# Performance work log

Measured on AMD Instinct MI355X. Metric: run time of the kernel, lower is better.

## Reference

```python
import jax, jax.numpy as jnp
import numpy as np

MIN_PTS = 4

def setup_inputs() -> dict:
    key = jax.random.key(0)
    ks = jax.random.split(key, 10)
    P, N = 2048, 256            # proposals, max points per proposal slot
    H1, H2, OUT = 64, 128, 256  # PointNet MLP widths, extractor out_dim
    points = jax.random.normal(ks[0], (P, N, 3), dtype=jnp.float32)
    lengths = jax.random.randint(ks[1], (P,), 0, N, dtype=jnp.int32)  # some < MIN_PTS -> invalid
    centers = jax.random.normal(ks[2], (P, 3), dtype=jnp.float32) * 10.0
    sizes = jax.random.uniform(ks[3], (P, 3), minval=0.5, maxval=4.0, dtype=jnp.float32)
    proposals = jnp.concatenate([centers, sizes], axis=1)  # (P, 6)
    def lin(k, fan_in, fan_out):
        return jax.random.normal(k, (fan_in, fan_out), dtype=jnp.float32) * np.float32(1.0 / np.sqrt(fan_in))
    return {
        'points': points, 'lengths': lengths, 'proposals': proposals,
        'W1': lin(ks[4], 3, H1),   'b1': jnp.zeros((H1,), jnp.float32),
        'W2': lin(ks[5], H1, H2),  'b2': jnp.zeros((H2,), jnp.float32),
        'W3': lin(ks[6], H2, OUT), 'b3': jnp.zeros((OUT,), jnp.float32),
        'Wc': lin(ks[7], OUT, 1),  'bc': jnp.zeros((1,), jnp.float32),
        'Wr': lin(ks[8], OUT, 4),  'br': jnp.zeros((4,), jnp.float32),
    }

def reference(points, lengths, proposals, W1, b1, W2, b2, W3, b3, Wc, bc, Wr, br):
    P, N, _ = points.shape
    # repeat-padding: point i of proposal p maps to index i % n_p (gather form of the torch loop)
    L = jnp.maximum(lengths, 1)
    idx = jnp.arange(N, dtype=lengths.dtype)[None, :] % L[:, None]          # (P, N)
    batched = jnp.take_along_axis(points, idx[:, :, None], axis=1)         # (P, N, 3)
    # MultiPositionExtractor: box-normalized coords -> pointwise MLP -> max-pool
    centers = proposals[:, :3]
    half = proposals[:, 3:] * 0.5 + 1e-6
    local = (batched - centers[:, None, :]) / half[:, None, :]             # (P, N, 3)
    h = jax.nn.relu(local @ W1 + b1)                                       # (P, N, 64)
    h = jax.nn.relu(h @ W2 + b2)                                           # (P, N, 128)
    h = jax.nn.relu(h @ W3 + b3)                                           # (P, N, 256)
    feats = jnp.max(h, axis=1)                                             # (P, 256)
    # scatter-back: proposals with < MIN_PTS points get zero feature vector
    valid = lengths >= MIN_PTS
    feats = jnp.where(valid[:, None], feats, jnp.zeros((), feats.dtype))
    cls_logits = feats @ Wc + bc                                           # (P, 1)
    reg_deltas = feats @ Wr + br                                           # (P, 4)
    return cls_logits, reg_deltas
```

## Files before the change

### kernel.cpp

```cpp
#include <hip/hip_runtime.h>
#include <hip/hip_bf16.h>

#define MIN_PTS 4

typedef short bf16x8 __attribute__((ext_vector_type(8)));
typedef float f32x4  __attribute__((ext_vector_type(4)));

__device__ __forceinline__ ushort f2bf(float x) {
    unsigned u = __float_as_uint(x);
    u = (u + 0x7fffu + ((u >> 16) & 1u)) >> 16;
    return (ushort)u;
}

__device__ __forceinline__ uint cvt_pk_bf16(float lo, float hi) {
    union { __hip_bfloat162 h; uint u; } cv;
    cv.h = __float22bfloat162_rn(make_float2(lo, hi));
    return cv.u;
}

__global__ void pack_weights(const float* __restrict__ W2, const float* __restrict__ W3,
                             ushort* __restrict__ B2P, ushort* __restrict__ B3P)
{
    int idx = blockIdx.x * 256 + threadIdx.x;
    if (idx < 8192) {
        int j = idx & 7, l = (idx >> 3) & 63, ks = (idx >> 9) & 1, nt = idx >> 10;
        int k   = ks * 32 + (l >> 4) * 8 + j;
        int col = nt * 16 + (l & 15);
        B2P[idx] = f2bf(W2[k * 128 + col]);
    }
    if (idx < 32768) {
        int j = idx & 7, l = (idx >> 3) & 63, ks = (idx >> 9) & 3, nt = idx >> 11;
        int k   = ks * 32 + (l >> 4) * 8 + j;
        int col = nt * 16 + (l & 15);
        B3P[idx] = f2bf(W3[k * 256 + col]);
    }
}

__global__ __launch_bounds__(512, 4) void refine_stripe128(
    const float* __restrict__ points,
    const int*   __restrict__ lengths,
    const float* __restrict__ proposals,
    const float* __restrict__ W1, const float* __restrict__ b1,
    const float* __restrict__ b2,
    const float* __restrict__ b3,
    const ushort* __restrict__ B2P, const ushort* __restrict__ B3P,
    int* __restrict__ featsG,
    int P, int N)
{
    const int bid = blockIdx.x;
    const int p   = bid >> 1;
    const int s   = bid & 1;
    const int len = lengths[p];
    if (len < MIN_PTS || s * 128 >= len) return;

    __shared__ __align__(16) ushort A1[8192];
    __shared__ __align__(16) ushort A3[16384];

    const int tid  = threadIdx.x;
    const int lane = tid & 63;
    const int wu   = __builtin_amdgcn_readfirstlane(tid >> 6);
    const int rc   = lane & 15;
    const int g    = lane >> 4;
    const int mtg  = wu >> 2;
    const int ntg  = wu & 3;

    const float cx = proposals[p * 6 + 0];
    const float cy = proposals[p * 6 + 1];
    const float cz = proposals[p * 6 + 2];
    const float rx = __builtin_amdgcn_rcpf(fmaf(proposals[p * 6 + 3], 0.5f, 1e-6f));
    const float ry = __builtin_amdgcn_rcpf(fmaf(proposals[p * 6 + 4], 0.5f, 1e-6f));
    const float rz = __builtin_amdgcn_rcpf(fmaf(proposals[p * 6 + 5], 0.5f, 1e-6f));

    {
        const int wp  = wu >> 1;
        const int pis = (wu & 1) * 64 + lane;
        const int jj  = min(s * 128 + pis, len - 1);
        const float* pt = points + ((long)p * N + jj) * 3;
        const float x0 = (pt[0] - cx) * rx;
        const float x1 = (pt[1] - cy) * ry;
        const float x2 = (pt[2] - cz) * rz;

        float v[16];
        #pragma unroll
        for (int i = 0; i < 16; ++i) {
            const int f = 16 * wp + i;
            v[i] = fmaxf(fmaf(x0, W1[f], fmaf(x1, W1[64 + f], fmaf(x2, W1[128 + f], b1[f]))), 0.f);
        }
        const int mt = pis >> 4;
        #pragma unroll
        for (int c = 0; c < 2; ++c) {
            uint4 qq;
            qq.x = cvt_pk_bf16(v[8 * c + 0], v[8 * c + 1]);
            qq.y = cvt_pk_bf16(v[8 * c + 2], v[8 * c + 3]);
            qq.z = cvt_pk_bf16(v[8 * c + 4], v[8 * c + 5]);
            qq.w = cvt_pk_bf16(v[8 * c + 6], v[8 * c + 7]);
            const int chunk = (mt * 2 + (wp >> 1)) * 64 + ((2 * wp + c) & 3) * 16 + rc;
            *(uint4*)&A1[chunk * 8] = qq;
        }
    }
    __syncthreads();

    {
        f32x4 acc2[4][2];
        #pragma unroll
        for (int nt = 0; nt < 2; ++nt) {
            f32x4 bq;
            #pragma unroll
            for (int rr = 0; rr < 4; ++rr) bq[rr] = b2[16 * (2 * ntg + nt) + 4 * g + rr];
            #pragma unroll
            for (int mt = 0; mt < 4; ++mt) acc2[mt][nt] = bq;
        }
        #pragma unroll
        for (int ks = 0; ks < 2; ++ks) {
            const bf16x8 bw0 = *(const bf16x8*)(B2P + (((2 * ntg + 0) * 2 + ks) * 64 + lane) * 8);
            const bf16x8 bw1 = *(const bf16x8*)(B2P + (((2 * ntg + 1) * 2 + ks) * 64 + lane) * 8);
            #pragma unroll
            for (int mt = 0; mt < 4; ++mt) {
                const bf16x8 a = *(const bf16x8*)&A1[(((4 * mtg + mt) * 2 + ks) * 64 + lane) * 8];
                acc2[mt][0] = __builtin_amdgcn_mfma_f32_16x16x32_bf16(bw0, a, acc2[mt][0], 0, 0, 0);
                acc2[mt][1] = __builtin_amdgcn_mfma_f32_16x16x32_bf16(bw1, a, acc2[mt][1], 0, 0, 0);
            }
        }
        #pragma unroll
        for (int mt = 0; mt < 4; ++mt)
            #pragma unroll
            for (int nt = 0; nt < 2; ++nt) {
                const uint u0 = cvt_pk_bf16(fmaxf(acc2[mt][nt][0], 0.f), fmaxf(acc2[mt][nt][1], 0.f));
                const uint u1 = cvt_pk_bf16(fmaxf(acc2[mt][nt][2], 0.f), fmaxf(acc2[mt][nt][3], 0.f));
                const int g3 = (2 * nt + (g >> 1)) & 3;
                const int chunk = ((4 * mtg + mt) * 4 + ntg) * 64 + g3 * 16 + rc;
                uint2 val; val.x = u0; val.y = u1;
                *(uint2*)&A3[chunk * 8 + (g & 1) * 4] = val;
            }
    }
    __syncthreads();

    {
        f32x4 acc3[4][4];
        #pragma unroll
        for (int nt = 0; nt < 4; ++nt) {
            const float bv = b3[16 * (4 * ntg + nt) + rc];
            #pragma unroll
            for (int mt = 0; mt < 4; ++mt)
                acc3[mt][nt] = (f32x4){bv, bv, bv, bv};
        }
        #pragma unroll
        for (int ks = 0; ks < 4; ++ks) {
            const bf16x8 b0 = *(const bf16x8*)(B3P + (((4 * ntg + 0) * 4 + ks) * 64 + lane) * 8);
            const bf16x8 b1f = *(const bf16x8*)(B3P + (((4 * ntg + 1) * 4 + ks) * 64 + lane) * 8);
            const bf16x8 b2f = *(const bf16x8*)(B3P + (((4 * ntg + 2) * 4 + ks) * 64 + lane) * 8);
            const bf16x8 b3f = *(const bf16x8*)(B3P + (((4 * ntg + 3) * 4 + ks) * 64 + lane) * 8);
            #pragma unroll
            for (int mt = 0; mt < 4; ++mt) {
                const bf16x8 a = *(const bf16x8*)&A3[(((4 * mtg + mt) * 4 + ks) * 64 + lane) * 8];
                acc3[mt][0] = __builtin_amdgcn_mfma_f32_16x16x32_bf16(a, b0,  acc3[mt][0], 0, 0, 0);
                acc3[mt][1] = __builtin_amdgcn_mfma_f32_16x16x32_bf16(a, b1f, acc3[mt][1], 0, 0, 0);
                acc3[mt][2] = __builtin_amdgcn_mfma_f32_16x16x32_bf16(a, b2f, acc3[mt][2], 0, 0, 0);
                acc3[mt][3] = __builtin_amdgcn_mfma_f32_16x16x32_bf16(a, b3f, acc3[mt][3], 0, 0, 0);
            }
        }
        float pool[4];
        #pragma unroll
        for (int nt = 0; nt < 4; ++nt) {
            float m = 0.f;
            #pragma unroll
            for (int mt = 0; mt < 4; ++mt)
                #pragma unroll
                for (int rr = 0; rr < 4; ++rr)
                    m = fmaxf(m, acc3[mt][nt][rr]);
            m = fmaxf(m, __shfl_xor(m, 16, 64));
            m = fmaxf(m, __shfl_xor(m, 32, 64));
            pool[nt] = m;
        }
        if (g == 0) {
            #pragma unroll
            for (int nt = 0; nt < 4; ++nt)
                atomicMax(&featsG[p * 256 + (4 * ntg + nt) * 16 + rc], __float_as_int(pool[nt]));
        }
    }
}

__global__ __launch_bounds__(256) void heads_kernel(
    const int* __restrict__ featsG,
    const float* __restrict__ Wc, const float* __restrict__ bc,
    const float* __restrict__ Wr, const float* __restrict__ br,
    float* __restrict__ out, int P)
{
    const int tid  = threadIdx.x;
    const int lane = tid & 63;
    const int p    = blockIdx.x * 4 + (tid >> 6);
    if (p >= P) return;

    const int4 vi = *(const int4*)&featsG[p * 256 + lane * 4];
    float v[4] = {__int_as_float(vi.x), __int_as_float(vi.y),
                  __int_as_float(vi.z), __int_as_float(vi.w)};

    const float4 wc = *(const float4*)&Wc[lane * 4];
    float c  = v[0] * wc.x + v[1] * wc.y + v[2] * wc.z + v[3] * wc.w;
    float r0 = 0.f, r1 = 0.f, r2 = 0.f, r3 = 0.f;
    #pragma unroll
    for (int i = 0; i < 4; ++i) {
        const float4 wr = *(const float4*)&Wr[(lane * 4 + i) * 4];
        r0 = fmaf(v[i], wr.x, r0);
        r1 = fmaf(v[i], wr.y, r1);
        r2 = fmaf(v[i], wr.z, r2);
        r3 = fmaf(v[i], wr.w, r3);
    }
    #pragma unroll
    for (int off = 32; off > 0; off >>= 1) {
        c  += __shfl_xor(c,  off, 64);
        r0 += __shfl_xor(r0, off, 64);
        r1 += __shfl_xor(r1, off, 64);
        r2 += __shfl_xor(r2, off, 64);
        r3 += __shfl_xor(r3, off, 64);
    }
    if (lane == 0) {
        out[p]             = c  + bc[0];
        out[P + p * 4 + 0] = r0 + br[0];
        out[P + p * 4 + 1] = r1 + br[1];
        out[P + p * 4 + 2] = r2 + br[2];
        out[P + p * 4 + 3] = r3 + br[3];
    }
}

extern "C" void kernel_launch(void* const* d_in, const int* in_sizes, int n_in,
                              void* d_out, int out_size, void* d_ws, size_t ws_size,
                              hipStream_t stream)
{
    const float* points    = (const float*)d_in[0];
    const int*   lengths   = (const int*)  d_in[1];
    const float* proposals = (const float*)d_in[2];
    const float* W1 = (const float*)d_in[3];
    const float* b1 = (const float*)d_in[4];
    const float* W2 = (const float*)d_in[5];
    const float* b2 = (const float*)d_in[6];
    const float* W3 = (const float*)d_in[7];
    const float* b3 = (const float*)d_in[8];
    const float* Wc = (const float*)d_in[9];
    const float* bc = (const float*)d_in[10];
    const float* Wr = (const float*)d_in[11];
    const float* br = (const float*)d_in[12];
    float* out = (float*)d_out;

    const int P = in_sizes[1];
    const int N = in_sizes[0] / (3 * P);
    const int S128 = (N + 127) / 128;

    ushort* B2P    = (ushort*)d_ws;
    ushort* B3P    = B2P + 8192;
    int*    featsG = (int*)((char*)d_ws + 81920);

    hipMemsetAsync(featsG, 0, (size_t)P * 256 * sizeof(int), stream);
    pack_weights<<<dim3(128), dim3(256), 0, stream>>>(W2, W3, B2P, B3P);
    refine_stripe128<<<dim3(P * S128), dim3(512), 0, stream>>>(
        points, lengths, proposals, W1, b1, b2, b3, B2P, B3P, featsG, P, N);
    heads_kernel<<<dim3((P + 3) / 4), dim3(256), 0, stream>>>(
        featsG, Wc, bc, Wr, br, out, P);
}
```

Baseline: 55.04 us.

## Keep MLP activations in registers per wave, removing shared memory and barriers

Restructures the fused PointNet kernel so each wavefront owns 64 points of a proposal and computes all three layers in registers. The layer-2 MFMA output layout is fed directly as the layer-3 A operand, made possible by permuting the K ordering when W3 is packed. The shared-memory staging buffers and both block barriers go away, and the grid becomes one 256-thread block per proposal. The cost is much higher register pressure, since all layer-2 activations stay live per wave. Layer 3 is now looped over column tiles, which re-reads the B3 weights from global or cache in every wave.

```diff
diff --git a/kernel.cpp b/kernel.cpp
--- a/kernel.cpp
+++ b/kernel.cpp
@@ -30,13 +30,13 @@
     }
     if (idx < 32768) {
         int j = idx & 7, l = (idx >> 3) & 63, ks = (idx >> 9) & 3, nt = idx >> 11;
-        int k   = ks * 32 + (l >> 4) * 8 + j;
+        int k   = 32 * ks + 16 * (j >> 2) + 4 * (l >> 4) + (j & 3);
         int col = nt * 16 + (l & 15);
         B3P[idx] = f2bf(W3[k * 256 + col]);
     }
 }
 
-__global__ __launch_bounds__(512, 4) void refine_stripe128(
+__global__ __launch_bounds__(256, 3) void refine_wave(
     const float* __restrict__ points,
     const int*   __restrict__ lengths,
     const float* __restrict__ proposals,
@@ -47,22 +47,17 @@
     int* __restrict__ featsG,
     int P, int N)
 {
-    const int bid = blockIdx.x;
-    const int p   = bid >> 1;
-    const int s   = bid & 1;
+    const int p   = blockIdx.x;
     const int len = lengths[p];
-    if (len < MIN_PTS || s * 128 >= len) return;
-
-    __shared__ __align__(16) ushort A1[8192];
-    __shared__ __align__(16) ushort A3[16384];
+    if (len < MIN_PTS) return;
 
     const int tid  = threadIdx.x;
+    const int s    = __builtin_amdgcn_readfirstlane(tid >> 6);
+    if (s * 64 >= len) return;
+
     const int lane = tid & 63;
-    const int wu   = __builtin_amdgcn_readfirstlane(tid >> 6);
     const int rc   = lane & 15;
     const int g    = lane >> 4;
-    const int mtg  = wu >> 2;
-    const int ntg  = wu & 3;
 
     const float cx = proposals[p * 6 + 0];
     const float cy = proposals[p * 6 + 1];
@@ -71,111 +66,107 @@
     const float ry = __builtin_amdgcn_rcpf(fmaf(proposals[p * 6 + 4], 0.5f, 1e-6f));
     const float rz = __builtin_amdgcn_rcpf(fmaf(proposals[p * 6 + 5], 0.5f, 1e-6f));
 
+    union U16 { uint u[4]; bf16x8 v; };
+
+    U16 a1[4][2];
     {
-        const int wp  = wu >> 1;
-        const int pis = (wu & 1) * 64 + lane;
-        const int jj  = min(s * 128 + pis, len - 1);
-        const float* pt = points + ((long)p * N + jj) * 3;
-        const float x0 = (pt[0] - cx) * rx;
-        const float x1 = (pt[1] - cy) * ry;
-        const float x2 = (pt[2] - cz) * rz;
-
-        float v[16];
-        #pragma unroll
-        for (int i = 0; i < 16; ++i) {
-            const int f = 16 * wp + i;
-            v[i] = fmaxf(fmaf(x0, W1[f], fmaf(x1, W1[64 + f], fmaf(x2, W1[128 + f], b1[f]))), 0.f);
-        }
-        const int mt = pis >> 4;
-        #pragma unroll
-        for (int c = 0; c < 2; ++c) {
-            uint4 qq;
-            qq.x = cvt_pk_bf16(v[8 * c + 0], v[8 * c + 1]);
-            qq.y = cvt_pk_bf16(v[8 * c + 2], v[8 * c + 3]);
-            qq.z = cvt_pk_bf16(v[8 * c + 4], v[8 * c + 5]);
-            qq.w = cvt_pk_bf16(v[8 * c + 6], v[8 * c + 7]);
-            const int chunk = (mt * 2 + (wp >> 1)) * 64 + ((2 * wp + c) & 3) * 16 + rc;
-            *(uint4*)&A1[chunk * 8] = qq;
-        }
-    }
-    __syncthreads();
-
-    {
-        f32x4 acc2[4][2];
-        #pragma unroll
-        for (int nt = 0; nt < 2; ++nt) {
-            f32x4 bq;
-            #pragma unroll
-            for (int rr = 0; rr < 4; ++rr) bq[rr] = b2[16 * (2 * ntg + nt) + 4 * g + rr];
-            #pragma unroll
-            for (int mt = 0; mt < 4; ++mt) acc2[mt][nt] = bq;
-        }
-        #pragma unroll
-        for (int ks = 0; ks < 2; ++ks) {
-            const bf16x8 bw0 = *(const bf16x8*)(B2P + (((2 * ntg + 0) * 2 + ks) * 64 + lane) * 8);
-            const bf16x8 bw1 = *(const bf16x8*)(B2P + (((2 * ntg + 1) * 2 + ks) * 64 + lane) * 8);
+        f32x4 wA[2][2], wB[2][2], wC[2][2], bV[2][2];
+        #pragma unroll
+        for (int ka = 0; ka < 2; ++ka) {
+            const int fb = 32 * ka + 8 * g;
+            wA[ka][0] = *(const f32x4*)&W1[fb];        wA[ka][1] = *(const f32x4*)&W1[fb + 4];
+            wB[ka][0] = *(const f32x4*)&W1[64 + fb];   wB[ka][1] = *(const f32x4*)&W1[64 + fb + 4];
+            wC[ka][0] = *(const f32x4*)&W1[128 + fb];  wC[ka][1] = *(const f32x4*)&W1[128 + fb + 4];
+            bV[ka][0] = *(const f32x4*)&b1[fb];        bV[ka][1] = *(const f32x4*)&b1[fb + 4];
+        }
+        const long pb = (long)p * N;
+        #pragma unroll
+        for (int mt = 0; mt < 4; ++mt) {
+            const int jj = min(s * 64 + mt * 16 + rc, len - 1);
+            const float* pt = points + (pb + jj) * 3;
+            const float x0 = (pt[0] - cx) * rx;
+            const float x1 = (pt[1] - cy) * ry;
+            const float x2 = (pt[2] - cz) * rz;
+            #pragma unroll
+            for (int ka = 0; ka < 2; ++ka) {
+                #pragma unroll
+                for (int h = 0; h < 2; ++h) {
+                    float v0 = fmaxf(fmaf(x0, wA[ka][h][0], fmaf(x1, wB[ka][h][0], fmaf(x2, wC[ka][h][0], bV[ka][h][0]))), 0.f);
+                    float v1 = fmaxf(fmaf(x0, wA[ka][h][1], fmaf(x1, wB[ka][h][1], fmaf(x2, wC[ka][h][1], bV[ka][h][1]))), 0.f);
+                    float v2 = fmaxf(fmaf(x0, wA[ka][h][2], fmaf(x1, wB[ka][h][2], fmaf(x2, wC[ka][h][2], bV[ka][h][2]))), 0.f);
+                    float v3 = fmaxf(fmaf(x0, wA[ka][h][3], fmaf(x1, wB[ka][h][3], fmaf(x2, wC[ka][h][3], bV[ka][h][3]))), 0.f);
+                    a1[mt][ka].u[2 * h + 0] = cvt_pk_bf16(v0, v1);
+                    a1[mt][ka].u[2 * h + 1] = cvt_pk_bf16(v2, v3);
+                }
+            }
+        }
+    }
+
+    U16 pa[4][4];
+    #pragma unroll
+    for (int ks3 = 0; ks3 < 4; ++ks3) {
+        f32x4 acc[2][4];
+        #pragma unroll
+        for (int n = 0; n < 2; ++n) {
+            const f32x4 bq = *(const f32x4*)&b2[16 * (2 * ks3 + n) + 4 * g];
+            #pragma unroll
+            for (int mt = 0; mt < 4; ++mt) acc[n][mt] = bq;
+        }
+        #pragma unroll
+        for (int kb = 0; kb < 2; ++kb) {
+            const bf16x8 bw0 = *(const bf16x8*)(B2P + (((2 * ks3 + 0) * 2 + kb) * 64 + lane) * 8);
+            const bf16x8 bw1 = *(const bf16x8*)(B2P + (((2 * ks3 + 1) * 2 + kb) * 64 + lane) * 8);
             #pragma unroll
             for (int mt = 0; mt < 4; ++mt) {
-                const bf16x8 a = *(const bf16x8*)&A1[(((4 * mtg + mt) * 2 + ks) * 64 + lane) * 8];
-                acc2[mt][0] = __builtin_amdgcn_mfma_f32_16x16x32_bf16(bw0, a, acc2[mt][0], 0, 0, 0);
-                acc2[mt][1] = __builtin_amdgcn_mfma_f32_16x16x32_bf16(bw1, a, acc2[mt][1], 0, 0, 0);
-            }
-        }
+                acc[0][mt] = __builtin_amdgcn_mfma_f32_16x16x32_bf16(bw0, a1[mt][kb].v, acc[0][mt], 0, 0, 0);
+                acc[1][mt] = __builtin_amdgcn_mfma_f32_16x16x32_bf16(bw1, a1[mt][kb].v, acc[1][mt], 0, 0, 0);
+            }
+        }
+        #pragma unroll
+        for (int mt = 0; mt < 4; ++mt) {
+            pa[ks3][mt].u[0] = cvt_pk_bf16(fmaxf(acc[0][mt][0], 0.f), fmaxf(acc[0][mt][1], 0.f));
+            pa[ks3][mt].u[1] = cvt_pk_bf16(fmaxf(acc[0][mt][2], 0.f), fmaxf(acc[0][mt][3], 0.f));
+            pa[ks3][mt].u[2] = cvt_pk_bf16(fmaxf(acc[1][mt][0], 0.f), fmaxf(acc[1][mt][1], 0.f));
+            pa[ks3][mt].u[3] = cvt_pk_bf16(fmaxf(acc[1][mt][2], 0.f), fmaxf(acc[1][mt][3], 0.f));
+        }
+    }
+
+    #pragma unroll 2
+    for (int c = 0; c < 8; ++c) {
+        const int nt0 = 2 * c, nt1 = 2 * c + 1;
+        const float bv0 = b3[16 * nt0 + rc];
+        const float bv1 = b3[16 * nt1 + rc];
+        f32x4 acc[2][4];
+        #pragma unroll
+        for (int mt = 0; mt < 4; ++mt) {
+            acc[0][mt] = (f32x4){bv0, bv0, bv0, bv0};
+            acc[1][mt] = (f32x4){bv1, bv1, bv1, bv1};
+        }
+        #pragma unroll
+        for (int ks = 0; ks < 4; ++ks) {
+            const bf16x8 f0 = *(const bf16x8*)(B3P + ((nt0 * 4 + ks) * 64 + lane) * 8);
+            const bf16x8 f1 = *(const bf16x8*)(B3P + ((nt1 * 4 + ks) * 64 + lane) * 8);
+            #pragma unroll
+            for (int mt = 0; mt < 4; ++mt) {
+                acc[0][mt] = __builtin_amdgcn_mfma_f32_16x16x32_bf16(pa[ks][mt].v, f0, acc[0][mt], 0, 0, 0);
+                acc[1][mt] = __builtin_amdgcn_mfma_f32_16x16x32_bf16(pa[ks][mt].v, f1, acc[1][mt], 0, 0, 0);
+            }
+        }
+        float p0 = 0.f, p1 = 0.f;
         #pragma unroll
         for (int mt = 0; mt < 4; ++mt)
             #pragma unroll
-            for (int nt = 0; nt < 2; ++nt) {
-                const uint u0 = cvt_pk_bf16(fmaxf(acc2[mt][nt][0], 0.f), fmaxf(acc2[mt][nt][1], 0.f));
-                const uint u1 = cvt_pk_bf16(fmaxf(acc2[mt][nt][2], 0.f), fmaxf(acc2[mt][nt][3], 0.f));
-                const int g3 = (2 * nt + (g >> 1)) & 3;
-                const int chunk = ((4 * mtg + mt) * 4 + ntg) * 64 + g3 * 16 + rc;
-                uint2 val; val.x = u0; val.y = u1;
-                *(uint2*)&A3[chunk * 8 + (g & 1) * 4] = val;
-            }
-    }
-    __syncthreads();
-
-    {
-        f32x4 acc3[4][4];
-        #pragma unroll
-        for (int nt = 0; nt < 4; ++nt) {
-            const float bv = b3[16 * (4 * ntg + nt) + rc];
-            #pragma unroll
-            for (int mt = 0; mt < 4; ++mt)
-                acc3[mt][nt] = (f32x4){bv, bv, bv, bv};
-        }
-        #pragma unroll
-        for (int ks = 0; ks < 4; ++ks) {
-            const bf16x8 b0 = *(const bf16x8*)(B3P + (((4 * ntg + 0) * 4 + ks) * 64 + lane) * 8);
-            const bf16x8 b1f = *(const bf16x8*)(B3P + (((4 * ntg + 1) * 4 + ks) * 64 + lane) * 8);
-            const bf16x8 b2f = *(const bf16x8*)(B3P + (((4 * ntg + 2) * 4 + ks) * 64 + lane) * 8);
-            const bf16x8 b3f = *(const bf16x8*)(B3P + (((4 * ntg + 3) * 4 + ks) * 64 + lane) * 8);
-            #pragma unroll
-            for (int mt = 0; mt < 4; ++mt) {
-                const bf16x8 a = *(const bf16x8*)&A3[(((4 * mtg + mt) * 4 + ks) * 64 + lane) * 8];
-                acc3[mt][0] = __builtin_amdgcn_mfma_f32_16x16x32_bf16(a, b0,  acc3[mt][0], 0, 0, 0);
-                acc3[mt][1] = __builtin_amdgcn_mfma_f32_16x16x32_bf16(a, b1f, acc3[mt][1], 0, 0, 0);
-                acc3[mt][2] = __builtin_amdgcn_mfma_f32_16x16x32_bf16(a, b2f, acc3[mt][2], 0, 0, 0);
-                acc3[mt][3] = __builtin_amdgcn_mfma_f32_16x16x32_bf16(a, b3f, acc3[mt][3], 0, 0, 0);
-            }
-        }
-        float pool[4];
-        #pragma unroll
-        for (int nt = 0; nt < 4; ++nt) {
-            float m = 0.f;
-            #pragma unroll
-            for (int mt = 0; mt < 4; ++mt)
-                #pragma unroll
-                for (int rr = 0; rr < 4; ++rr)
-                    m = fmaxf(m, acc3[mt][nt][rr]);
-            m = fmaxf(m, __shfl_xor(m, 16, 64));
-            m = fmaxf(m, __shfl_xor(m, 32, 64));
-            pool[nt] = m;
-        }
+            for (int rr = 0; rr < 4; ++rr) {
+                p0 = fmaxf(p0, acc[0][mt][rr]);
+                p1 = fmaxf(p1, acc[1][mt][rr]);
+            }
+        p0 = fmaxf(p0, __shfl_xor(p0, 16, 64));
+        p0 = fmaxf(p0, __shfl_xor(p0, 32, 64));
+        p1 = fmaxf(p1, __shfl_xor(p1, 16, 64));
+        p1 = fmaxf(p1, __shfl_xor(p1, 32, 64));
         if (g == 0) {
-            #pragma unroll
-            for (int nt = 0; nt < 4; ++nt)
-                atomicMax(&featsG[p * 256 + (4 * ntg + nt) * 16 + rc], __float_as_int(pool[nt]));
+            atomicMax(&featsG[p * 256 + nt0 * 16 + rc], __float_as_int(p0));
+            atomicMax(&featsG[p * 256 + nt1 * 16 + rc], __float_as_int(p1));
         }
     }
 }
@@ -244,7 +235,6 @@
 
     const int P = in_sizes[1];
     const int N = in_sizes[0] / (3 * P);
-    const int S128 = (N + 127) / 128;
 
     ushort* B2P    = (ushort*)d_ws;
     ushort* B3P    = B2P + 8192;
@@ -252,7 +242,7 @@
 
     hipMemsetAsync(featsG, 0, (size_t)P * 256 * sizeof(int), stream);
     pack_weights<<<dim3(128), dim3(256), 0, stream>>>(W2, W3, B2P, B3P);
-    refine_stripe128<<<dim3(P * S128), dim3(512), 0, stream>>>(
+    refine_wave<<<dim3(P), dim3(256), 0, stream>>>(
         points, lengths, proposals, W1, b1, b2, b3, B2P, B3P, featsG, P, N);
     heads_kernel<<<dim3((P + 3) / 4), dim3(256), 0, stream>>>(
         featsG, Wc, bc, Wr, br, out, P);
```

After: 54.28 us. No clear change (-1.4%).
